# Kernel optimization log

Hardware: AMD Instinct MI355X
Metric: run time of the kernel (lower is better)

Reference implementation:

```python
import jax, jax.numpy as jnp
import numpy as np

NUM_HEADS = 16
HIDDEN = 1024
HEAD_DIM = HIDDEN // NUM_HEADS
B, S, D = 2, 2048, 1024


def setup_inputs() -> dict:
    key = jax.random.key(0)
    ks = jax.random.split(key, 7)
    scale = 1.0 / np.sqrt(D)
    return {
        "query": jax.random.normal(ks[0], (B, S, D), dtype=jnp.float32),
        "key": jax.random.normal(ks[1], (B, S, D), dtype=jnp.float32),
        "value": jax.random.normal(ks[2], (B, S, D), dtype=jnp.float32),
        "Wk_w": jax.random.normal(ks[3], (HIDDEN, D), dtype=jnp.float32) * scale,
        "Wk_b": jax.random.normal(ks[4], (HIDDEN,), dtype=jnp.float32) * scale,
        "Wv_w": jax.random.normal(ks[5], (HIDDEN, D), dtype=jnp.float32) * scale,
        "Wv_b": jax.random.normal(ks[6], (HIDDEN,), dtype=jnp.float32) * scale,
    }


def reference(query, key, value, Wk_w, Wk_b, Wv_w, Wv_b):
    # NOTE: in the original torch module, self.W_v is assigned twice, so the
    # SAME Linear (Wv) projects both key and value; Wk projects query.
    b, s, _ = query.shape

    def split_heads(x):  # [b,s,hidden] -> [b,h,s,hd]
        return x.reshape(b, s, NUM_HEADS, HEAD_DIM).transpose(0, 2, 1, 3)

    q = split_heads(query @ Wk_w.T + Wk_b)
    k = split_heads(key @ Wv_w.T + Wv_b)
    v = split_heads(value @ Wv_w.T + Wv_b)

    scores = jnp.einsum("bhqd,bhkd->bhqk", q, k) / jnp.sqrt(
        jnp.asarray(HEAD_DIM, dtype=q.dtype))
    probs = jax.nn.softmax(scores, axis=-1)
    out = jnp.einsum("bhqk,bhkd->bhqd", probs, v)
    return out.transpose(0, 2, 1, 3).reshape(b, s, NUM_HEADS * HEAD_DIM)
```

## Files before the change

### kernel.cpp

```cpp
#include <hip/hip_runtime.h>
#include <stdint.h>

typedef unsigned short u16;
typedef uint32_t u32;
typedef __bf16 bf16x8 __attribute__((ext_vector_type(8)));
typedef float f32x4 __attribute__((ext_vector_type(4)));
typedef float f32x16 __attribute__((ext_vector_type(16)));
typedef u16 u16x4 __attribute__((ext_vector_type(4)));
typedef u16 u16x8 __attribute__((ext_vector_type(8)));

#define XQ_OFF 0ul
#define XK_OFF 4194304ul
#define XV_OFF 8388608ul
#define WK_OFF 12582912ul
#define WV_OFF 13631488ul
#define Q_OFF  14680064ul
#define K_OFF  18874368ul
#define V_OFF  23068672ul

#define SCQ 0.18033688011112042f

#if __has_builtin(__builtin_amdgcn_exp2f)
#define EXP2F(x) __builtin_amdgcn_exp2f(x)
#else
#define EXP2F(x) exp2f(x)
#endif

__device__ __forceinline__ u16 f2bf(float f) {
  u32 u = __float_as_uint(f);
  u32 r = (u + 0x7fffu + ((u >> 16) & 1u)) >> 16;
  return (u16)r;
}

__device__ __forceinline__ u32 pk2(float a, float b) {
  typedef __bf16 bf2_t __attribute__((ext_vector_type(2)));
  typedef float f2_t __attribute__((ext_vector_type(2)));
  f2_t v; v[0] = a; v[1] = b;
  bf2_t h = __builtin_convertvector(v, bf2_t);
  union { bf2_t h; u32 u; } cv; cv.h = h; return cv.u;
}

__device__ __forceinline__ void load_lds16(const void* g, void* l) {
  __builtin_amdgcn_global_load_lds(
      (const __attribute__((address_space(1))) u32*)g,
      (__attribute__((address_space(3))) u32*)l, 16, 0, 0);
}

__global__ __launch_bounds__(256) void cvt_tile_kernel(
    const float* __restrict__ xq, const float* __restrict__ xk,
    const float* __restrict__ xv, const float* __restrict__ wk,
    const float* __restrict__ wv, u16* __restrict__ ws) {
  __shared__ u16 tile[4096];
  const int bid = blockIdx.x;
  const float* src; size_t dstbase; int rt, ktp;
  if (bid < 3072) {
    int m = bid >> 10, loc = bid & 1023;
    src = (m == 0) ? xq : (m == 1) ? xk : xv;
    dstbase = (size_t)m * 4194304ul;
    rt = loc >> 4; ktp = loc & 15;
  } else {
    int r2 = bid - 3072;
    int m = r2 >> 8, loc = r2 & 255;
    src = m ? wv : wk;
    dstbase = WK_OFF + (size_t)m * 1048576ul;
    rt = loc >> 4; ktp = loc & 15;
  }
  const int t = threadIdx.x;
  const int row0 = t >> 4, c = t & 15;
  const int k = c * 4;
  const float* s = src + (size_t)(rt * 64 + row0) * 1024ul + ktp * 64 + k;
#pragma unroll
  for (int i = 0; i < 4; ++i) {
    float4 v = *(const float4*)(s + (size_t)i * 16384ul);
    int row = row0 + i * 16;
    u32* p = (u32*)(tile + ((k >> 5) * 2048 + ((k >> 3) & 3) * 512 + row * 8 + (k & 7)));
    p[0] = pk2(v.x, v.y);
    p[1] = pk2(v.z, v.w);
  }
  __syncthreads();
  u16* dst = ws + dstbase + (size_t)(rt * 32 + ktp * 2) * 2048ul;
#pragma unroll
  for (int so = 0; so < 4096; so += 2048)
    *(u16x8*)(dst + so + t * 8) = *(const u16x8*)(tile + so + t * 8);
}

__global__ __launch_bounds__(256, 3) void proj_kernel(u16* __restrict__ ws,
                                                      const float* __restrict__ bk,
                                                      const float* __restrict__ bv) {
  const int proj = blockIdx.z;
  const int mtile = blockIdx.x;
  const int ntile = blockIdx.y;
  const u16* A = ws + (size_t)proj * 4194304ul;
  const u16* Bw = ws + ((proj == 0) ? WK_OFF : WV_OFF);
  const float* bias = (proj == 0) ? bk : bv;
  u16* outQ = ws + Q_OFF;
  u16* outK = ws + K_OFF;
  u16* outV = ws + V_OFF;

  const int t = threadIdx.x;
  const int w = t >> 6, lane = t & 63;
  const int wm = w >> 1, wn = w & 1;
  const int c32 = lane & 31, g2 = lane >> 5;

  const u16* Aw = A + (size_t)(2 * mtile + wm) * 65536ul + (size_t)g2 * 512ul + (size_t)c32 * 8ul;
  const u16* Bb = Bw + (size_t)(2 * ntile + wn) * 65536ul + (size_t)g2 * 512ul + (size_t)c32 * 8ul;

  f32x16 acc[2][2];
#pragma unroll
  for (int rf = 0; rf < 2; ++rf)
#pragma unroll
    for (int cf = 0; cf < 2; ++cf)
#pragma unroll
      for (int i = 0; i < 16; ++i) acc[rf][cf][i] = 0.f;

  bf16x8 ab[4][2], bb[4][2];
#pragma unroll
  for (int s = 0; s < 4; ++s)
#pragma unroll
    for (int f = 0; f < 2; ++f) {
      ab[s][f] = *(const bf16x8*)(Aw + (size_t)s * 1024ul + f * 256);
      bb[s][f] = *(const bf16x8*)(Bb + (size_t)s * 1024ul + f * 256);
    }

#pragma unroll 1
  for (int ks = 0; ks < 60; ks += 4) {
#pragma unroll
    for (int s = 0; s < 4; ++s) {
#pragma unroll
      for (int rf = 0; rf < 2; ++rf)
#pragma unroll
        for (int cf = 0; cf < 2; ++cf)
          acc[rf][cf] =
              __builtin_amdgcn_mfma_f32_32x32x16_bf16(ab[s][rf], bb[s][cf], acc[rf][cf], 0, 0, 0);
      const size_t o = (size_t)(ks + 4 + s) * 1024ul;
#pragma unroll
      for (int f = 0; f < 2; ++f) {
        ab[s][f] = *(const bf16x8*)(Aw + o + f * 256);
        bb[s][f] = *(const bf16x8*)(Bb + o + f * 256);
      }
    }
  }
#pragma unroll
  for (int s = 0; s < 4; ++s)
#pragma unroll
    for (int rf = 0; rf < 2; ++rf)
#pragma unroll
      for (int cf = 0; cf < 2; ++cf)
        acc[rf][cf] =
            __builtin_amdgcn_mfma_f32_32x32x16_bf16(ab[s][rf], bb[s][cf], acc[rf][cf], 0, 0, 0);

  const int m0w = mtile * 128 + wm * 64, n0w = ntile * 128 + wn * 64;
#pragma unroll
  for (int cf = 0; cf < 2; ++cf) {
    const int col = n0w + cf * 32 + c32;
    const float bvv = bias[col];
    const int h = col >> 6, d = col & 63;
#pragma unroll
    for (int rf = 0; rf < 2; ++rf) {
#pragma unroll
      for (int q = 0; q < 4; ++q) {
        const int mbase = m0w + rf * 32 + q * 8 + g2 * 4;
        const int b = mbase >> 11;
        const int bh = b * 16 + h;
        if (proj == 2) {
          const int s = mbase & 2047;
          u16x4 pk;
#pragma unroll
          for (int r = 0; r < 4; ++r) pk[r] = f2bf(acc[rf][cf][q * 4 + r] + bvv);
          size_t idx = (size_t)bh * 131072ul + (size_t)(s >> 6) * 4096ul +
                       (size_t)((s & 63) >> 3) * 512ul + (size_t)d * 8ul + (size_t)(s & 7);
          *(u16x4*)(outV + idx) = pk;
        } else {
          u16* dst = (proj == 0) ? outQ : outK;
#pragma unroll
          for (int r = 0; r < 4; ++r) {
            const int m = mbase + r;
            const int s = m & 2047;
            float y = acc[rf][cf][q * 4 + r] + bvv;
            if (proj == 0) y *= SCQ;
            size_t idx;
            if (proj == 0)
              idx = (size_t)bh * 131072ul + (size_t)(s >> 7) * 8192ul + (size_t)(d >> 3) * 1024ul +
                    (size_t)(s & 127) * 8ul + (size_t)(d & 7);
            else
              idx = (size_t)bh * 131072ul + (size_t)(s >> 6) * 4096ul + (size_t)(d >> 3) * 512ul +
                    (size_t)(s & 63) * 8ul + (size_t)(d & 7);
            dst[idx] = f2bf(y);
          }
        }
      }
    }
  }
}

__global__ __launch_bounds__(256, 2) void attn_kernel(const u16* __restrict__ ws,
                                                      float* __restrict__ out) {
  const int bh = blockIdx.x, qtile = blockIdx.y;
  const int b = bh >> 4, h = bh & 15;
  const int t = threadIdx.x, w = t >> 6, lane = t & 63, g = lane >> 4, c = lane & 15;

  __shared__ __align__(16) u16 Ps[4][1280];

  const u16* Qg = ws + Q_OFF + (size_t)bh * 131072ul + (size_t)qtile * 8192ul;
  const u16* Kg = ws + K_OFF + (size_t)bh * 131072ul;
  const u16* Vg = ws + V_OFF + (size_t)bh * 131072ul;

  bf16x8 qf[2][2];
#pragma unroll
  for (int ntq = 0; ntq < 2; ++ntq)
#pragma unroll
    for (int ks = 0; ks < 2; ++ks)
      qf[ntq][ks] = *(const bf16x8*)(Qg + (ks * 4 + g) * 1024 + (w * 32 + ntq * 16 + c) * 8);

  u16x8 ou;
#pragma unroll
  for (int i = 0; i < 8; ++i) ou[i] = (u16)0x3F80;
  union { u16x8 u; bf16x8 b; } ocv; ocv.u = ou;
  const bf16x8 onesf = ocv.b;

  f32x4 O[2][4], Lacc[2];
#pragma unroll
  for (int mtq = 0; mtq < 2; ++mtq) {
    Lacc[mtq] = (f32x4){0.f, 0.f, 0.f, 0.f};
#pragma unroll
    for (int nt = 0; nt < 4; ++nt) O[mtq][nt] = (f32x4){0.f, 0.f, 0.f, 0.f};
  }

  u16* Psw = Ps[w];

  bf16x8 kf[2][4];
#pragma unroll
  for (int ks = 0; ks < 2; ++ks)
#pragma unroll
    for (int mtk = 0; mtk < 4; ++mtk)
      kf[ks][mtk] = *(const bf16x8*)(Kg + (ks * 4 + g) * 512 + (mtk * 16 + c) * 8);

#pragma unroll 1
  for (int j = 0; j < 32; ++j) {
    const u16* Vj = Vg + (size_t)j * 4096ul;
    bf16x8 vf[2][4];
#pragma unroll
    for (int ksh = 0; ksh < 2; ++ksh)
#pragma unroll
      for (int nt = 0; nt < 4; ++nt)
        vf[ksh][nt] = *(const bf16x8*)(Vj + (ksh * 4 + g) * 512 + (nt * 16 + c) * 8);

    f32x4 St[4][2];
#pragma unroll
    for (int mtk = 0; mtk < 4; ++mtk)
#pragma unroll
      for (int ntq = 0; ntq < 2; ++ntq) St[mtk][ntq] = (f32x4){0.f, 0.f, 0.f, 0.f};
#pragma unroll
    for (int ks = 0; ks < 2; ++ks)
#pragma unroll
      for (int mtk = 0; mtk < 4; ++mtk)
#pragma unroll
        for (int ntq = 0; ntq < 2; ++ntq)
          St[mtk][ntq] =
              __builtin_amdgcn_mfma_f32_16x16x32_bf16(kf[ks][mtk], qf[ntq][ks], St[mtk][ntq], 0, 0, 0);

    const u16* Kn = Kg + (size_t)((j < 31) ? (j + 1) : 31) * 4096ul;
#pragma unroll
    for (int ks = 0; ks < 2; ++ks)
#pragma unroll
      for (int mtk = 0; mtk < 4; ++mtk)
        kf[ks][mtk] = *(const bf16x8*)(Kn + (ks * 4 + g) * 512 + (mtk * 16 + c) * 8);

#pragma unroll
    for (int mtk = 0; mtk < 4; ++mtk)
#pragma unroll
      for (int ntq = 0; ntq < 2; ++ntq)
#pragma unroll
        for (int r = 0; r < 4; ++r) St[mtk][ntq][r] = EXP2F(St[mtk][ntq][r]);

#pragma unroll
    for (int ksh = 0; ksh < 2; ++ksh) {
#pragma unroll
      for (int ntq = 0; ntq < 2; ++ntq)
#pragma unroll
        for (int m2 = 0; m2 < 2; ++m2) {
          const int mtk = ksh * 2 + m2;
          u32 lo = pk2(St[mtk][ntq][0], St[mtk][ntq][1]);
          u32 hi = pk2(St[mtk][ntq][2], St[mtk][ntq][3]);
          u32* p = (u32*)(Psw + (ntq * 16 + c) * 40 + m2 * 16 + g * 4);
          p[0] = lo; p[1] = hi;
        }
      asm volatile("s_waitcnt lgkmcnt(0)" ::: "memory");
      bf16x8 pf[2];
#pragma unroll
      for (int mtq = 0; mtq < 2; ++mtq)
        pf[mtq] = *(const bf16x8*)(Psw + (mtq * 16 + c) * 40 + g * 8);
#pragma unroll
      for (int mtq = 0; mtq < 2; ++mtq) {
        Lacc[mtq] = __builtin_amdgcn_mfma_f32_16x16x32_bf16(pf[mtq], onesf, Lacc[mtq], 0, 0, 0);
#pragma unroll
        for (int nt = 0; nt < 4; ++nt)
          O[mtq][nt] =
              __builtin_amdgcn_mfma_f32_16x16x32_bf16(pf[mtq], vf[ksh][nt], O[mtq][nt], 0, 0, 0);
      }
    }
  }

  const int q0 = qtile * 128 + w * 32;
#pragma unroll
  for (int mtq = 0; mtq < 2; ++mtq)
#pragma unroll
    for (int r = 0; r < 4; ++r) {
      const float inv = 1.0f / Lacc[mtq][r];
      const int q = q0 + mtq * 16 + g * 4 + r;
      float* rowp = out + (size_t)(b * 2048 + q) * 1024ul + h * 64;
#pragma unroll
      for (int nt = 0; nt < 4; ++nt) rowp[nt * 16 + c] = O[mtq][nt][r] * inv;
    }
}

extern "C" void kernel_launch(void* const* d_in, const int* in_sizes, int n_in,
                              void* d_out, int out_size, void* d_ws, size_t ws_size,
                              hipStream_t stream) {
  const float* q = (const float*)d_in[0];
  const float* k = (const float*)d_in[1];
  const float* v = (const float*)d_in[2];
  const float* wk = (const float*)d_in[3];
  const float* bk = (const float*)d_in[4];
  const float* wv = (const float*)d_in[5];
  const float* bv = (const float*)d_in[6];
  u16* ws = (u16*)d_ws;
  float* out = (float*)d_out;

  cvt_tile_kernel<<<3584, 256, 0, stream>>>(q, k, v, wk, wv, ws);
  proj_kernel<<<dim3(32, 8, 3), 256, 0, stream>>>(ws, bk, bv);
  attn_kernel<<<dim3(32, 16), 256, 0, stream>>>(ws, out);
}
```

Measured before the change: 180.0 us.

## Stage projection GEMM through swizzled LDS and double-buffer V loads in attention

The projection kernel now stages A and B tiles into double-buffered, XOR-swizzled LDS using global_load_lds and computes with 16x16x32 MFMAs, replacing per-wave direct global register loads with 32x32 MFMAs. This lets the waves of a block share operand tiles and overlaps the next tile's load with compute. The attention loop is unrolled by two with ping-pong V register buffers so the next V block is prefetched a step ahead, and s_setprio is raised around MFMA bursts. The changes add a __syncthreads per k-step and more registers for the extra V buffer.

```diff
diff --git a/kernel.cpp b/kernel.cpp
--- a/kernel.cpp
+++ b/kernel.cpp
@@ -5,7 +5,6 @@
 typedef uint32_t u32;
 typedef __bf16 bf16x8 __attribute__((ext_vector_type(8)));
 typedef float f32x4 __attribute__((ext_vector_type(4)));
-typedef float f32x16 __attribute__((ext_vector_type(16)));
 typedef u16 u16x4 __attribute__((ext_vector_type(4)));
 typedef u16 u16x8 __attribute__((ext_vector_type(8)));
 
@@ -44,6 +43,10 @@
   __builtin_amdgcn_global_load_lds(
       (const __attribute__((address_space(1))) u32*)g,
       (__attribute__((address_space(3))) u32*)l, 16, 0, 0);
+}
+
+__device__ __forceinline__ u32 swz(u32 L) {
+  return L ^ (((L >> 7) & 1u) << 4) ^ (((L >> 10) & 3u) << 5);
 }
 
 __global__ __launch_bounds__(256) void cvt_tile_kernel(
@@ -100,96 +103,172 @@
   const int t = threadIdx.x;
   const int w = t >> 6, lane = t & 63;
   const int wm = w >> 1, wn = w & 1;
-  const int c32 = lane & 31, g2 = lane >> 5;
-
-  const u16* Aw = A + (size_t)(2 * mtile + wm) * 65536ul + (size_t)g2 * 512ul + (size_t)c32 * 8ul;
-  const u16* Bb = Bw + (size_t)(2 * ntile + wn) * 65536ul + (size_t)g2 * 512ul + (size_t)c32 * 8ul;
-
-  f32x16 acc[2][2];
-#pragma unroll
-  for (int rf = 0; rf < 2; ++rf)
-#pragma unroll
-    for (int cf = 0; cf < 2; ++cf)
-#pragma unroll
-      for (int i = 0; i < 16; ++i) acc[rf][cf][i] = 0.f;
-
-  bf16x8 ab[4][2], bb[4][2];
-#pragma unroll
-  for (int s = 0; s < 4; ++s)
-#pragma unroll
-    for (int f = 0; f < 2; ++f) {
-      ab[s][f] = *(const bf16x8*)(Aw + (size_t)s * 1024ul + f * 256);
-      bb[s][f] = *(const bf16x8*)(Bb + (size_t)s * 1024ul + f * 256);
-    }
+  const int g = lane >> 4, c = lane & 15;
+
+  __shared__ __align__(16) u16 As[2][2][2048];
+  __shared__ __align__(16) u16 Bs[2][2][2048];
+
+  const u16* Ag = A + (size_t)(2 * mtile) * 65536ul;
+  const u16* Bg = Bw + (size_t)(2 * ntile) * 65536ul;
+  const u32 t8 = (u32)t * 8u;
+  const u32 so = swz((u32)t * 16u) >> 1;
+
+  u32 poff[4];
+#pragma unroll
+  for (int mt = 0; mt < 4; ++mt)
+    poff[mt] = swz((u32)((g << 10) | ((mt * 16 + c) << 4))) >> 1;
+
+#define PSTAGE(buf, kt)                                            \
+  do {                                                             \
+    const size_t ko = (size_t)(kt) * 2048ul + so;                  \
+    load_lds16(Ag + ko, &As[buf][0][t8]);                          \
+    load_lds16(Ag + 65536ul + ko, &As[buf][1][t8]);                \
+    load_lds16(Bg + ko, &Bs[buf][0][t8]);                          \
+    load_lds16(Bg + 65536ul + ko, &Bs[buf][1][t8]);                \
+  } while (0)
+
+  f32x4 acc[4][4];
+#pragma unroll
+  for (int mt = 0; mt < 4; ++mt)
+#pragma unroll
+    for (int nt = 0; nt < 4; ++nt) acc[mt][nt] = (f32x4){0.f, 0.f, 0.f, 0.f};
+
+  PSTAGE(0, 0);
+  __syncthreads();
 
 #pragma unroll 1
-  for (int ks = 0; ks < 60; ks += 4) {
-#pragma unroll
-    for (int s = 0; s < 4; ++s) {
-#pragma unroll
-      for (int rf = 0; rf < 2; ++rf)
-#pragma unroll
-        for (int cf = 0; cf < 2; ++cf)
-          acc[rf][cf] =
-              __builtin_amdgcn_mfma_f32_32x32x16_bf16(ab[s][rf], bb[s][cf], acc[rf][cf], 0, 0, 0);
-      const size_t o = (size_t)(ks + 4 + s) * 1024ul;
-#pragma unroll
-      for (int f = 0; f < 2; ++f) {
-        ab[s][f] = *(const bf16x8*)(Aw + o + f * 256);
-        bb[s][f] = *(const bf16x8*)(Bb + o + f * 256);
-      }
-    }
-  }
-#pragma unroll
-  for (int s = 0; s < 4; ++s)
-#pragma unroll
-    for (int rf = 0; rf < 2; ++rf)
-#pragma unroll
-      for (int cf = 0; cf < 2; ++cf)
-        acc[rf][cf] =
-            __builtin_amdgcn_mfma_f32_32x32x16_bf16(ab[s][rf], bb[s][cf], acc[rf][cf], 0, 0, 0);
-
-  const int m0w = mtile * 128 + wm * 64, n0w = ntile * 128 + wn * 64;
-#pragma unroll
-  for (int cf = 0; cf < 2; ++cf) {
-    const int col = n0w + cf * 32 + c32;
+  for (int kt = 0; kt < 32; ++kt) {
+    const int cur = kt & 1;
+    if (kt < 31) PSTAGE(cur ^ 1, kt + 1);
+    const u16* Ap = As[cur][wm];
+    const u16* Bp = Bs[cur][wn];
+    bf16x8 af[4], bfv[4];
+#pragma unroll
+    for (int mt = 0; mt < 4; ++mt) af[mt] = *(const bf16x8*)(Ap + poff[mt]);
+#pragma unroll
+    for (int nt = 0; nt < 4; ++nt) bfv[nt] = *(const bf16x8*)(Bp + poff[nt]);
+#pragma unroll
+    for (int mt = 0; mt < 4; ++mt)
+#pragma unroll
+      for (int nt = 0; nt < 4; ++nt)
+        acc[mt][nt] =
+            __builtin_amdgcn_mfma_f32_16x16x32_bf16(af[mt], bfv[nt], acc[mt][nt], 0, 0, 0);
+    __syncthreads();
+  }
+#undef PSTAGE
+
+  const int m0 = mtile * 128 + wm * 64;
+  const int n0 = ntile * 128 + wn * 64;
+#pragma unroll
+  for (int nt = 0; nt < 4; ++nt) {
+    const int col = n0 + nt * 16 + c;
     const float bvv = bias[col];
     const int h = col >> 6, d = col & 63;
 #pragma unroll
-    for (int rf = 0; rf < 2; ++rf) {
-#pragma unroll
-      for (int q = 0; q < 4; ++q) {
-        const int mbase = m0w + rf * 32 + q * 8 + g2 * 4;
-        const int b = mbase >> 11;
-        const int bh = b * 16 + h;
-        if (proj == 2) {
-          const int s = mbase & 2047;
-          u16x4 pk;
-#pragma unroll
-          for (int r = 0; r < 4; ++r) pk[r] = f2bf(acc[rf][cf][q * 4 + r] + bvv);
-          size_t idx = (size_t)bh * 131072ul + (size_t)(s >> 6) * 4096ul +
-                       (size_t)((s & 63) >> 3) * 512ul + (size_t)d * 8ul + (size_t)(s & 7);
-          *(u16x4*)(outV + idx) = pk;
-        } else {
-          u16* dst = (proj == 0) ? outQ : outK;
-#pragma unroll
-          for (int r = 0; r < 4; ++r) {
-            const int m = mbase + r;
-            const int s = m & 2047;
-            float y = acc[rf][cf][q * 4 + r] + bvv;
-            if (proj == 0) y *= SCQ;
-            size_t idx;
-            if (proj == 0)
-              idx = (size_t)bh * 131072ul + (size_t)(s >> 7) * 8192ul + (size_t)(d >> 3) * 1024ul +
-                    (size_t)(s & 127) * 8ul + (size_t)(d & 7);
-            else
-              idx = (size_t)bh * 131072ul + (size_t)(s >> 6) * 4096ul + (size_t)(d >> 3) * 512ul +
-                    (size_t)(s & 63) * 8ul + (size_t)(d & 7);
-            dst[idx] = f2bf(y);
-          }
+    for (int mt = 0; mt < 4; ++mt) {
+      const int mbase = m0 + mt * 16 + g * 4;
+      const int b = mbase >> 11;
+      const int bh = b * 16 + h;
+      const int s = mbase & 2047;
+      if (proj == 2) {
+        u16x4 pk;
+#pragma unroll
+        for (int r = 0; r < 4; ++r) pk[r] = f2bf(acc[mt][nt][r] + bvv);
+        size_t idx = (size_t)bh * 131072ul + (size_t)(s >> 6) * 4096ul +
+                     (size_t)((s & 63) >> 3) * 512ul + (size_t)d * 8ul + (size_t)(s & 7);
+        *(u16x4*)(outV + idx) = pk;
+      } else {
+        u16* dst = (proj == 0) ? outQ : outK;
+#pragma unroll
+        for (int r = 0; r < 4; ++r) {
+          const int m = mbase + r;
+          const int s2 = m & 2047;
+          float y = acc[mt][nt][r] + bvv;
+          if (proj == 0) y *= SCQ;
+          size_t idx;
+          if (proj == 0)
+            idx = (size_t)bh * 131072ul + (size_t)(s2 >> 7) * 8192ul + (size_t)(d >> 3) * 1024ul +
+                  (size_t)(s2 & 127) * 8ul + (size_t)(d & 7);
+          else
+            idx = (size_t)bh * 131072ul + (size_t)(s2 >> 6) * 4096ul + (size_t)(d >> 3) * 512ul +
+                  (size_t)(s2 & 63) * 8ul + (size_t)(d & 7);
+          dst[idx] = f2bf(y);
         }
       }
     }
+  }
+}
+
+__device__ __forceinline__ void attn_step(
+    int jj, const u16* __restrict__ Kg, const u16* __restrict__ Vg,
+    bf16x8 (&kf)[2][4], bf16x8 (&vcur)[2][4], bf16x8 (&vnxt)[2][4],
+    const bf16x8 (&qf)[2][2], const bf16x8 onesf, f32x4 (&O)[2][4],
+    f32x4 (&Lacc)[2], u16* __restrict__ Psw, int g, int c) {
+  const int jn = (jj < 31) ? jj + 1 : 31;
+  const u16* Vn = Vg + (size_t)jn * 4096ul;
+#pragma unroll
+  for (int ksh = 0; ksh < 2; ++ksh)
+#pragma unroll
+    for (int nt = 0; nt < 4; ++nt)
+      vnxt[ksh][nt] = *(const bf16x8*)(Vn + (ksh * 4 + g) * 512 + (nt * 16 + c) * 8);
+
+  f32x4 St[4][2];
+#pragma unroll
+  for (int mtk = 0; mtk < 4; ++mtk)
+#pragma unroll
+    for (int ntq = 0; ntq < 2; ++ntq) St[mtk][ntq] = (f32x4){0.f, 0.f, 0.f, 0.f};
+  __builtin_amdgcn_s_setprio(1);
+#pragma unroll
+  for (int ks = 0; ks < 2; ++ks)
+#pragma unroll
+    for (int mtk = 0; mtk < 4; ++mtk)
+#pragma unroll
+      for (int ntq = 0; ntq < 2; ++ntq)
+        St[mtk][ntq] =
+            __builtin_amdgcn_mfma_f32_16x16x32_bf16(kf[ks][mtk], qf[ntq][ks], St[mtk][ntq], 0, 0, 0);
+  __builtin_amdgcn_s_setprio(0);
+
+  const u16* Kn = Kg + (size_t)jn * 4096ul;
+#pragma unroll
+  for (int ks = 0; ks < 2; ++ks)
+#pragma unroll
+    for (int mtk = 0; mtk < 4; ++mtk)
+      kf[ks][mtk] = *(const bf16x8*)(Kn + (ks * 4 + g) * 512 + (mtk * 16 + c) * 8);
+
+#pragma unroll
+  for (int mtk = 0; mtk < 4; ++mtk)
+#pragma unroll
+    for (int ntq = 0; ntq < 2; ++ntq)
+#pragma unroll
+      for (int r = 0; r < 4; ++r) St[mtk][ntq][r] = EXP2F(St[mtk][ntq][r]);
+
+#pragma unroll
+  for (int ksh = 0; ksh < 2; ++ksh) {
+#pragma unroll
+    for (int ntq = 0; ntq < 2; ++ntq)
+#pragma unroll
+      for (int m2 = 0; m2 < 2; ++m2) {
+        const int mtk = ksh * 2 + m2;
+        u32 lo = pk2(St[mtk][ntq][0], St[mtk][ntq][1]);
+        u32 hi = pk2(St[mtk][ntq][2], St[mtk][ntq][3]);
+        u32* p = (u32*)(Psw + (ntq * 16 + c) * 40 + m2 * 16 + g * 4);
+        p[0] = lo; p[1] = hi;
+      }
+    asm volatile("s_waitcnt lgkmcnt(0)" ::: "memory");
+    bf16x8 pf[2];
+#pragma unroll
+    for (int mtq = 0; mtq < 2; ++mtq)
+      pf[mtq] = *(const bf16x8*)(Psw + (mtq * 16 + c) * 40 + g * 8);
+    __builtin_amdgcn_s_setprio(1);
+#pragma unroll
+    for (int mtq = 0; mtq < 2; ++mtq) {
+      Lacc[mtq] = __builtin_amdgcn_mfma_f32_16x16x32_bf16(pf[mtq], onesf, Lacc[mtq], 0, 0, 0);
+#pragma unroll
+      for (int nt = 0; nt < 4; ++nt)
+        O[mtq][nt] =
+            __builtin_amdgcn_mfma_f32_16x16x32_bf16(pf[mtq], vcur[ksh][nt], O[mtq][nt], 0, 0, 0);
+    }
+    __builtin_amdgcn_s_setprio(0);
   }
 }
 
@@ -234,71 +313,17 @@
 #pragma unroll
     for (int mtk = 0; mtk < 4; ++mtk)
       kf[ks][mtk] = *(const bf16x8*)(Kg + (ks * 4 + g) * 512 + (mtk * 16 + c) * 8);
+  bf16x8 vfA[2][4], vfB[2][4];
+#pragma unroll
+  for (int ksh = 0; ksh < 2; ++ksh)
+#pragma unroll
+    for (int nt = 0; nt < 4; ++nt)
+      vfA[ksh][nt] = *(const bf16x8*)(Vg + (ksh * 4 + g) * 512 + (nt * 16 + c) * 8);
 
 #pragma unroll 1
-  for (int j = 0; j < 32; ++j) {
-    const u16* Vj = Vg + (size_t)j * 4096ul;
-    bf16x8 vf[2][4];
-#pragma unroll
-    for (int ksh = 0; ksh < 2; ++ksh)
-#pragma unroll
-      for (int nt = 0; nt < 4; ++nt)
-        vf[ksh][nt] = *(const bf16x8*)(Vj + (ksh * 4 + g) * 512 + (nt * 16 + c) * 8);
-
-    f32x4 St[4][2];
-#pragma unroll
-    for (int mtk = 0; mtk < 4; ++mtk)
-#pragma unroll
-      for (int ntq = 0; ntq < 2; ++ntq) St[mtk][ntq] = (f32x4){0.f, 0.f, 0.f, 0.f};
-#pragma unroll
-    for (int ks = 0; ks < 2; ++ks)
-#pragma unroll
-      for (int mtk = 0; mtk < 4; ++mtk)
-#pragma unroll
-        for (int ntq = 0; ntq < 2; ++ntq)
-          St[mtk][ntq] =
-              __builtin_amdgcn_mfma_f32_16x16x32_bf16(kf[ks][mtk], qf[ntq][ks], St[mtk][ntq], 0, 0, 0);
-
-    const u16* Kn = Kg + (size_t)((j < 31) ? (j + 1) : 31) * 4096ul;
-#pragma unroll
-    for (int ks = 0; ks < 2; ++ks)
-#pragma unroll
-      for (int mtk = 0; mtk < 4; ++mtk)
-        kf[ks][mtk] = *(const bf16x8*)(Kn + (ks * 4 + g) * 512 + (mtk * 16 + c) * 8);
-
-#pragma unroll
-    for (int mtk = 0; mtk < 4; ++mtk)
-#pragma unroll
-      for (int ntq = 0; ntq < 2; ++ntq)
-#pragma unroll
-        for (int r = 0; r < 4; ++r) St[mtk][ntq][r] = EXP2F(St[mtk][ntq][r]);
-
-#pragma unroll
-    for (int ksh = 0; ksh < 2; ++ksh) {
-#pragma unroll
-      for (int ntq = 0; ntq < 2; ++ntq)
-#pragma unroll
-        for (int m2 = 0; m2 < 2; ++m2) {
-          const int mtk = ksh * 2 + m2;
-          u32 lo = pk2(St[mtk][ntq][0], St[mtk][ntq][1]);
-          u32 hi = pk2(St[mtk][ntq][2], St[mtk][ntq][3]);
-          u32* p = (u32*)(Psw + (ntq * 16 + c) * 40 + m2 * 16 + g * 4);
-          p[0] = lo; p[1] = hi;
-        }
-      asm volatile("s_waitcnt lgkmcnt(0)" ::: "memory");
-      bf16x8 pf[2];
-#pragma unroll
-      for (int mtq = 0; mtq < 2; ++mtq)
-        pf[mtq] = *(const bf16x8*)(Psw + (mtq * 16 + c) * 40 + g * 8);
-#pragma unroll
-      for (int mtq = 0; mtq < 2; ++mtq) {
-        Lacc[mtq] = __builtin_amdgcn_mfma_f32_16x16x32_bf16(pf[mtq], onesf, Lacc[mtq], 0, 0, 0);
-#pragma unroll
-        for (int nt = 0; nt < 4; ++nt)
-          O[mtq][nt] =
-              __builtin_amdgcn_mfma_f32_16x16x32_bf16(pf[mtq], vf[ksh][nt], O[mtq][nt], 0, 0, 0);
-      }
-    }
+  for (int j2 = 0; j2 < 16; ++j2) {
+    attn_step(2 * j2, Kg, Vg, kf, vfA, vfB, qf, onesf, O, Lacc, Psw, g, c);
+    attn_step(2 * j2 + 1, Kg, Vg, kf, vfB, vfA, qf, onesf, O, Lacc, Psw, g, c);
   }
 
   const int q0 = qtile * 128 + w * 32;
```

Result: no change. 180.3 us (+0.1%).
